# Performance work log

Hardware: AMD Instinct MI355X
Metric: run time of the kernel (lower is better)

## Reference

```python
import jax, jax.numpy as jnp
import numpy as np
from jax import lax

N_FREE = 10
DT = 0.1
COMP = 4


def setup_inputs() -> dict:
    key = jax.random.key(0)
    kx, kw = jax.random.split(key)
    B, D = 256, 16384
    nodes = D // COMP  # 4096
    x = jax.random.normal(kx, (B, D), dtype=jnp.float32)
    # Hopfield-style node-coupling matrix (learned parameter), small init for stable relaxation
    W = jax.random.normal(kw, (nodes, nodes), dtype=jnp.float32) * 0.02
    return {"x": x, "W": W}


def reference(x, W):
    B, D = x.shape
    nodes = D // COMP
    # project scalar features to multivectors (B, nodes, comp)
    x_mv = x.reshape(B, nodes, COMP)
    W_sym = 0.5 * (W + W.T)  # symmetric coupling => well-defined energy

    def step(h, _):
        rho = jnp.tanh(h)                                      # (B, nodes, comp)
        drive = jnp.einsum('nm,bmc->bnc', W_sym, rho) + x_mv   # recurrent + input coupling
        grad_E = h - (1.0 - rho * rho) * drive                 # dE/dh
        return h - DT * grad_E, None

    h_free, _ = lax.scan(step, x_mv, None, length=N_FREE)
    return h_free[..., 0]  # scalar (grade-0) component, (B, nodes)
```

## Files before the change

### kernel.cpp

```cpp
#include <hip/hip_runtime.h>
#include <hip/hip_bf16.h>


#define NODES 4096
#define KDIM  4096
#define MDIM  1024
#define DLEN  16384
#define HALF_ELEMS 4194304

typedef __attribute__((ext_vector_type(8))) __bf16 bf16x8;
typedef __attribute__((ext_vector_type(8))) unsigned short u16x8;
typedef __attribute__((ext_vector_type(4))) unsigned short u16x4;
typedef __attribute__((ext_vector_type(4))) float  f32x4;

static __device__ __forceinline__ unsigned short f32_to_bf16(float f) {
    unsigned int u = __float_as_uint(f);
    u += 0x7fffu + ((u >> 16) & 1u);
    return (unsigned short)(u >> 16);
}
static __device__ __forceinline__ float bf16_to_f32(unsigned short u) {
    return __uint_as_float(((unsigned int)u) << 16);
}

__global__ __launch_bounds__(256)
void symw_kernel(const float* __restrict__ W, unsigned short* __restrict__ Wbp) {
    __shared__ float Ta[64][64];
    __shared__ float Tb[64][65];
    const int tn = blockIdx.y, tm = blockIdx.x;
    const int c  = threadIdx.x & 63;
    const int r0 = threadIdx.x >> 6;
#pragma unroll
    for (int rr = 0; rr < 16; ++rr) {
        int r = r0 * 16 + rr;
        Ta[r][c] = W[(size_t)(tn * 64 + r) * 4096 + tm * 64 + c];
        Tb[r][c] = W[(size_t)(tm * 64 + r) * 4096 + tn * 64 + c];
    }
    __syncthreads();
#pragma unroll
    for (int rr = 0; rr < 16; ++rr) {
        int r = r0 * 16 + rr;
        float v = 0.5f * (Ta[r][c] + Tb[c][r]);
        int n = tn * 64 + r;
        int k = tm * 64 + c;
        size_t addr = ((size_t)(k >> 5) * 256 + (n >> 4)) * 512
                    + (size_t)((n & 15) | (((k >> 3) & 3) << 4)) * 8 + (k & 7);
        Wbp[addr] = f32_to_bf16(v);
    }
}

__global__ __launch_bounds__(256)
void init_kernel(const float* __restrict__ x,
                 unsigned short* __restrict__ hb,
                 unsigned short* __restrict__ xb,
                 unsigned short* __restrict__ P0) {
    int idx = blockIdx.x * blockDim.x + threadIdx.x;
    int b = idx >> 12;
    int m = idx & 4095;
    f32x4 xv = *(const f32x4*)(x + (size_t)idx * 4);
    u16x4 xq;
#pragma unroll
    for (int c = 0; c < 4; ++c) xq[c] = f32_to_bf16(xv[c]);
    *(u16x4*)(xb + (size_t)idx * 4) = xq;
    *(u16x4*)(hb + (size_t)idx * 4) = xq;
    size_t base = ((size_t)(m >> 5) * 64 + (b >> 2)) * 512
                + (size_t)((m >> 3) & 3) * 128 + (m & 7);
#pragma unroll
    for (int c = 0; c < 4; ++c) {
        P0[base + (size_t)((b & 3) * 4 + c) * 8] = f32_to_bf16(tanhf(xv[c]));
    }
}

__global__ __launch_bounds__(256, 2)
void gemm_kernel(const unsigned short* __restrict__ Pcur,
                 const unsigned short* __restrict__ Wbp,
                 unsigned short* __restrict__ Dp) {
    __shared__ unsigned short Bs[4 * 4096];

    const int id   = blockIdx.x;
    const int bx   = (id & 7) * 4 + ((id >> 3) & 3);
    const int by   = (id >> 5) & 7;
    const int ks   = id >> 8;
    const int T0   = ks * 64;

    const int tid  = threadIdx.x;
    const int w    = tid >> 6;
    const int lane = tid & 63;
    const int wm   = w >> 1;
    const int wn   = w & 1;

    size_t soff[2]; int dsto[2];
#pragma unroll
    for (int j = 0; j < 2; ++j) {
        int c = tid + 256 * j;
        soff[j] = ((size_t)(bx * 8 + (c >> 6))) * 512 + (size_t)(c & 63) * 8;
        dsto[j] = c * 8;
    }
    size_t aoff[4];
#pragma unroll
    for (int mi = 0; mi < 4; ++mi)
        aoff[mi] = ((size_t)(by * 8 + wm * 4 + mi)) * 512 + (size_t)lane * 8;
    const int boff = (wn * 4) * 512 + lane * 8;

    f32x4 acc[4][4];
#pragma unroll
    for (int mi = 0; mi < 4; ++mi)
#pragma unroll
        for (int ni = 0; ni < 4; ++ni)
            acc[mi][ni] = (f32x4){0.f, 0.f, 0.f, 0.f};

    bf16x8 aA[4], aB[4];

#define TC(t) ((t) < 63 ? (t) : 63)

#define STAGE(slot, tl)                                                         \
    do {                                                                        \
        const unsigned short* src = Wbp + (size_t)(T0 + (tl)) * 131072;         \
        _Pragma("unroll")                                                       \
        for (int j = 0; j < 2; ++j) {                                           \
            __builtin_amdgcn_global_load_lds(                                   \
                (const __attribute__((address_space(1))) void*)(src + soff[j]), \
                (__attribute__((address_space(3))) void*)                      \
                    (Bs + (slot) * 4096 + dsto[j]),                             \
                16, 0, 0);                                                      \
        }                                                                       \
    } while (0)

#define LOADA(s, tl)                                                            \
    do {                                                                        \
        const unsigned short* Pt = Pcur + (size_t)(T0 + (tl)) * 32768;          \
        _Pragma("unroll")                                                       \
        for (int mi = 0; mi < 4; ++mi)                                          \
            s[mi] = *(const bf16x8*)(Pt + aoff[mi]);                            \
    } while (0)

#define COMPUTE(slot, s)                                                        \
    do {                                                                        \
        const unsigned short* Bb = Bs + (slot) * 4096;                          \
        bf16x8 bfr[4];                                                          \
        _Pragma("unroll")                                                       \
        for (int ni = 0; ni < 4; ++ni)                                          \
            bfr[ni] = *(const bf16x8*)(Bb + boff + ni * 512);                   \
        _Pragma("unroll")                                                       \
        for (int mi = 0; mi < 4; ++mi)                                          \
            _Pragma("unroll")                                                   \
            for (int ni = 0; ni < 4; ++ni)                                      \
                acc[mi][ni] = __builtin_amdgcn_mfma_f32_16x16x32_bf16(          \
                    s[mi], bfr[ni], acc[mi][ni], 0, 0, 0);                      \
    } while (0)

    STAGE(0, 0);
    LOADA(aA, 0);
    STAGE(1, 1);
    STAGE(2, 2);
    LOADA(aB, 1);
    STAGE(3, 3);
    asm volatile("s_waitcnt vmcnt(10)" ::: "memory");
    __builtin_amdgcn_s_barrier();
    COMPUTE(0, aA);

    for (int tp = 0; tp < 31; ++tp) {
        const int t = 1 + 2 * tp;
        LOADA(aA, TC(t + 1));
        STAGE((t + 3) & 3, TC(t + 3));
        asm volatile("s_waitcnt vmcnt(10)" ::: "memory");
        __builtin_amdgcn_s_barrier();
        COMPUTE(t & 3, aB);

        const int u = t + 1;
        LOADA(aB, TC(u + 1));
        STAGE((u + 3) & 3, TC(u + 3));
        asm volatile("s_waitcnt vmcnt(10)" ::: "memory");
        __builtin_amdgcn_s_barrier();
        COMPUTE(u & 3, aA);
    }
    asm volatile("s_waitcnt vmcnt(0)" ::: "memory");
    __builtin_amdgcn_s_barrier();
    COMPUTE(3, aB);
#undef STAGE
#undef LOADA
#undef COMPUTE
#undef TC

    const int lr = lane & 15, lk = lane >> 4;
    unsigned short* D = Dp + (size_t)ks * HALF_ELEMS;
#pragma unroll
    for (int mi = 0; mi < 4; ++mi) {
        int i0 = by * 128 + wm * 64 + mi * 16 + lk * 4;
#pragma unroll
        for (int ni = 0; ni < 4; ++ni) {
            int n = bx * 128 + wn * 64 + ni * 16 + lr;
#pragma unroll
            for (int r = 0; r < 4; ++r)
                D[(size_t)(i0 + r) * NODES + n] = f32_to_bf16(acc[mi][ni][r]);
        }
    }
}

__global__ __launch_bounds__(256)
void combine_kernel(const unsigned short* __restrict__ Dp,
                    const unsigned short* __restrict__ xb,
                    unsigned short* __restrict__ hb,
                    unsigned short* __restrict__ Pnxt,
                    float* __restrict__ out) {
    int g  = blockIdx.x * 256 + threadIdx.x;
    int b  = g >> 9;
    int mg = (g & 511) << 3;
    size_t ebase = (size_t)b * DLEN + (size_t)mg * 4;

    u16x8 hw[4], xw[4];
#pragma unroll
    for (int j = 0; j < 4; ++j) {
        hw[j] = *(const u16x8*)(hb + ebase + j * 8);
        xw[j] = *(const u16x8*)(xb + ebase + j * 8);
    }
    u16x8 d0[4], d1[4];
#pragma unroll
    for (int c = 0; c < 4; ++c) {
        size_t off = (size_t)(b * 4 + c) * NODES + mg;
        d0[c] = *(const u16x8*)(Dp + off);
        d1[c] = *(const u16x8*)(Dp + HALF_ELEMS + off);
    }
    u16x8 pn[4];
    float o[8];
#pragma unroll
    for (int j = 0; j < 4; ++j) {
        u16x8 hnw;
#pragma unroll
        for (int s = 0; s < 8; ++s) {
            int c = s & 3;
            int e = j * 2 + (s >> 2);
            float hv   = bf16_to_f32(hw[j][s]);
            float xv   = bf16_to_f32(xw[j][s]);
            float p    = bf16_to_f32(d0[c][e]) + bf16_to_f32(d1[c][e]);
            float rho  = tanhf(hv);
            float drive = p + xv;
            float hnew = 0.9f * hv + 0.1f * (1.0f - rho * rho) * drive;
            hnw[s] = f32_to_bf16(hnew);
            pn[c][e] = f32_to_bf16(tanhf(hnew));
            if (c == 0) o[e] = hnew;
        }
        hw[j] = hnw;
    }
    if (Pnxt) {
#pragma unroll
        for (int j = 0; j < 4; ++j)
            *(u16x8*)(hb + ebase + j * 8) = hw[j];
#pragma unroll
        for (int c = 0; c < 4; ++c) {
            size_t pa = (size_t)(mg >> 5) * 32768 + (size_t)(b >> 2) * 512
                      + (size_t)(((b & 3) * 4 + c) | (((mg >> 3) & 3) << 4)) * 8;
            *(u16x8*)(Pnxt + pa) = pn[c];
        }
    }
    if (out) {
        *(f32x4*)(out + (size_t)b * NODES + mg)     = (f32x4){o[0], o[1], o[2], o[3]};
        *(f32x4*)(out + (size_t)b * NODES + mg + 4) = (f32x4){o[4], o[5], o[6], o[7]};
    }
}

extern "C" void kernel_launch(void* const* d_in, const int* in_sizes, int n_in,
                              void* d_out, int out_size, void* d_ws, size_t ws_size,
                              hipStream_t stream) {
    const float* x = (const float*)d_in[0];
    const float* W = (const float*)d_in[1];
    float* out = (float*)d_out;

    char* ws = (char*)d_ws;
    unsigned short* Wbp = (unsigned short*)(ws);
    unsigned short* P0  = (unsigned short*)(ws + ((size_t)32 << 20));
    unsigned short* P1  = (unsigned short*)(ws + ((size_t)40 << 20));
    unsigned short* hb  = (unsigned short*)(ws + ((size_t)48 << 20));
    unsigned short* xb  = (unsigned short*)(ws + ((size_t)56 << 20));
    unsigned short* Dp  = (unsigned short*)(ws + ((size_t)64 << 20));

    symw_kernel<<<dim3(64, 64), 256, 0, stream>>>(W, Wbp);
    init_kernel<<<dim3(4096), 256, 0, stream>>>(x, hb, xb, P0);

    unsigned short* pc = P0;
    unsigned short* pn = P1;
    for (int s = 0; s < 10; ++s) {
        gemm_kernel<<<dim3(512), 256, 0, stream>>>(pc, Wbp, Dp);
        combine_kernel<<<dim3(512), 256, 0, stream>>>(
            Dp, xb, hb, (s == 9) ? nullptr : pn, (s == 9) ? out : nullptr);
        unsigned short* t = pc; pc = pn; pn = t;
    }
}
```

Measured before the change: 550.5 us.

## Double k-tile per pipeline stage in GEMM and halve symmetrization work

The GEMM now stages two 32-wide K slices per shared-memory slot (64 KB of LDS across 4 slots), which halves the number of barrier/wait iterations and reorders the pipeline so each barrier comes before the next stage issue. Separately, symw_kernel processes only upper-triangle tile pairs and writes both the tile and its transpose, cutting redundant W reads. The larger LDS footprint may reduce occupancy below the two blocks per CU that the launch bounds request, and the new vmcnt counts must match the per-stage load totals exactly.

```diff
diff --git a/kernel.cpp b/kernel.cpp
--- a/kernel.cpp
+++ b/kernel.cpp
@@ -22,11 +22,17 @@
     return __uint_as_float(((unsigned int)u) << 16);
 }
 
+static __device__ __forceinline__ size_t wbp_addr(int n, int k) {
+    return ((size_t)(k >> 5) * 256 + (n >> 4)) * 512
+         + (size_t)((n & 15) | (((k >> 3) & 3) << 4)) * 8 + (k & 7);
+}
+
 __global__ __launch_bounds__(256)
 void symw_kernel(const float* __restrict__ W, unsigned short* __restrict__ Wbp) {
-    __shared__ float Ta[64][64];
+    const int tn = blockIdx.y, tm = blockIdx.x;
+    if (tm < tn) return;
+    __shared__ float Ta[64][65];
     __shared__ float Tb[64][65];
-    const int tn = blockIdx.y, tm = blockIdx.x;
     const int c  = threadIdx.x & 63;
     const int r0 = threadIdx.x >> 6;
 #pragma unroll
@@ -40,11 +46,15 @@
     for (int rr = 0; rr < 16; ++rr) {
         int r = r0 * 16 + rr;
         float v = 0.5f * (Ta[r][c] + Tb[c][r]);
-        int n = tn * 64 + r;
-        int k = tm * 64 + c;
-        size_t addr = ((size_t)(k >> 5) * 256 + (n >> 4)) * 512
-                    + (size_t)((n & 15) | (((k >> 3) & 3) << 4)) * 8 + (k & 7);
-        Wbp[addr] = f32_to_bf16(v);
+        Wbp[wbp_addr(tn * 64 + r, tm * 64 + c)] = f32_to_bf16(v);
+    }
+    if (tm != tn) {
+#pragma unroll
+        for (int rr = 0; rr < 16; ++rr) {
+            int r = r0 * 16 + rr;
+            float v = 0.5f * (Tb[r][c] + Ta[c][r]);
+            Wbp[wbp_addr(tm * 64 + r, tn * 64 + c)] = f32_to_bf16(v);
+        }
     }
 }
 
@@ -74,13 +84,13 @@
 void gemm_kernel(const unsigned short* __restrict__ Pcur,
                  const unsigned short* __restrict__ Wbp,
                  unsigned short* __restrict__ Dp) {
-    __shared__ unsigned short Bs[4 * 4096];
+    __shared__ unsigned short Bs[4 * 8192];
 
     const int id   = blockIdx.x;
     const int bx   = (id & 7) * 4 + ((id >> 3) & 3);
     const int by   = (id >> 5) & 7;
     const int ks   = id >> 8;
-    const int T0   = ks * 64;
+    const int K32_0 = ks * 64;
 
     const int tid  = threadIdx.x;
     const int w    = tid >> 6;
@@ -88,11 +98,14 @@
     const int wm   = w >> 1;
     const int wn   = w & 1;
 
-    size_t soff[2]; int dsto[2];
-#pragma unroll
-    for (int j = 0; j < 2; ++j) {
-        int c = tid + 256 * j;
-        soff[j] = ((size_t)(bx * 8 + (c >> 6))) * 512 + (size_t)(c & 63) * 8;
+    size_t soff[4]; int dsto[4];
+#pragma unroll
+    for (int j = 0; j < 4; ++j) {
+        int c  = tid + 256 * j;
+        int f  = c >> 6;
+        int kf = f >> 3, nf = f & 7;
+        soff[j] = (size_t)kf * 131072
+                + ((size_t)(bx * 8 + nf)) * 512 + (size_t)(c & 63) * 8;
         dsto[j] = c * 8;
     }
     size_t aoff[4];
@@ -108,74 +121,70 @@
         for (int ni = 0; ni < 4; ++ni)
             acc[mi][ni] = (f32x4){0.f, 0.f, 0.f, 0.f};
 
-    bf16x8 aA[4], aB[4];
-
-#define TC(t) ((t) < 63 ? (t) : 63)
+    bf16x8 aA[4][2], aB[4][2];
+
+#define TC(t) ((t) < 31 ? (t) : 31)
 
 #define STAGE(slot, tl)                                                         \
     do {                                                                        \
-        const unsigned short* src = Wbp + (size_t)(T0 + (tl)) * 131072;         \
+        const unsigned short* src = Wbp + (size_t)(K32_0 + 2 * (tl)) * 131072;  \
         _Pragma("unroll")                                                       \
-        for (int j = 0; j < 2; ++j) {                                           \
+        for (int j = 0; j < 4; ++j) {                                           \
             __builtin_amdgcn_global_load_lds(                                   \
                 (const __attribute__((address_space(1))) void*)(src + soff[j]), \
                 (__attribute__((address_space(3))) void*)                      \
-                    (Bs + (slot) * 4096 + dsto[j]),                             \
+                    (Bs + (slot) * 8192 + dsto[j]),                             \
                 16, 0, 0);                                                      \
         }                                                                       \
     } while (0)
 
 #define LOADA(s, tl)                                                            \
     do {                                                                        \
-        const unsigned short* Pt = Pcur + (size_t)(T0 + (tl)) * 32768;          \
-        _Pragma("unroll")                                                       \
-        for (int mi = 0; mi < 4; ++mi)                                          \
-            s[mi] = *(const bf16x8*)(Pt + aoff[mi]);                            \
-    } while (0)
-
-#define COMPUTE(slot, s)                                                        \
-    do {                                                                        \
-        const unsigned short* Bb = Bs + (slot) * 4096;                          \
-        bf16x8 bfr[4];                                                          \
-        _Pragma("unroll")                                                       \
-        for (int ni = 0; ni < 4; ++ni)                                          \
-            bfr[ni] = *(const bf16x8*)(Bb + boff + ni * 512);                   \
+        const unsigned short* Pt = Pcur + (size_t)(K32_0 + 2 * (tl)) * 32768;   \
         _Pragma("unroll")                                                       \
         for (int mi = 0; mi < 4; ++mi)                                          \
             _Pragma("unroll")                                                   \
+            for (int kk = 0; kk < 2; ++kk)                                      \
+                s[mi][kk] = *(const bf16x8*)(Pt + (size_t)kk * 32768 + aoff[mi]); \
+    } while (0)
+
+#define COMPUTE(slot, s)                                                        \
+    do {                                                                        \
+        const unsigned short* Bb = Bs + (slot) * 8192;                          \
+        _Pragma("unroll")                                                       \
+        for (int kk = 0; kk < 2; ++kk) {                                        \
+            bf16x8 bfr[4];                                                      \
+            _Pragma("unroll")                                                   \
             for (int ni = 0; ni < 4; ++ni)                                      \
-                acc[mi][ni] = __builtin_amdgcn_mfma_f32_16x16x32_bf16(          \
-                    s[mi], bfr[ni], acc[mi][ni], 0, 0, 0);                      \
+                bfr[ni] = *(const bf16x8*)(Bb + boff + (kk * 8 + ni) * 512);    \
+            _Pragma("unroll")                                                   \
+            for (int mi = 0; mi < 4; ++mi)                                      \
+                _Pragma("unroll")                                               \
+                for (int ni = 0; ni < 4; ++ni)                                  \
+                    acc[mi][ni] = __builtin_amdgcn_mfma_f32_16x16x32_bf16(      \
+                        s[mi][kk], bfr[ni], acc[mi][ni], 0, 0, 0);              \
+        }                                                                       \
     } while (0)
 
     STAGE(0, 0);
-    LOADA(aA, 0);
     STAGE(1, 1);
     STAGE(2, 2);
-    LOADA(aB, 1);
-    STAGE(3, 3);
-    asm volatile("s_waitcnt vmcnt(10)" ::: "memory");
-    __builtin_amdgcn_s_barrier();
-    COMPUTE(0, aA);
-
-    for (int tp = 0; tp < 31; ++tp) {
-        const int t = 1 + 2 * tp;
-        LOADA(aA, TC(t + 1));
+    LOADA(aA, 0);
+
+    for (int tp = 0; tp < 16; ++tp) {
+        const int t = 2 * tp;
+        if (t == 0) { asm volatile("s_waitcnt vmcnt(16)" ::: "memory"); }
+        else        { asm volatile("s_waitcnt vmcnt(12)" ::: "memory"); }
+        __builtin_amdgcn_s_barrier();
         STAGE((t + 3) & 3, TC(t + 3));
-        asm volatile("s_waitcnt vmcnt(10)" ::: "memory");
+        LOADA(aB, TC(t + 1));
+        COMPUTE(t & 3, aA);
+        asm volatile("s_waitcnt vmcnt(12)" ::: "memory");
         __builtin_amdgcn_s_barrier();
-        COMPUTE(t & 3, aB);
-
-        const int u = t + 1;
-        LOADA(aB, TC(u + 1));
-        STAGE((u + 3) & 3, TC(u + 3));
-        asm volatile("s_waitcnt vmcnt(10)" ::: "memory");
-        __builtin_amdgcn_s_barrier();
-        COMPUTE(u & 3, aA);
-    }
-    asm volatile("s_waitcnt vmcnt(0)" ::: "memory");
-    __builtin_amdgcn_s_barrier();
-    COMPUTE(3, aB);
+        STAGE((t + 4) & 3, TC(t + 4));
+        LOADA(aA, TC(t + 2));
+        COMPUTE((t + 1) & 3, aB);
+    }
 #undef STAGE
 #undef LOADA
 #undef COMPUTE
```

Result: faster. 538.1 us (-2.3%).
